# Performance work log

Hardware: AMD Instinct MI355X
Metric: run time of the kernel (lower is better)

Reference implementation:

```python
import jax, jax.numpy as jnp
import numpy as np
from jax import lax

FS = 250
FREQS = np.arange(1.0, 41.0)  # 40 frequencies, 1..40 Hz
NCH = 32
NCYC = 6.0

def _kernel_size():
    f_min = float(FREQS.min())
    cyc = max(2.0, NCYC * (f_min / 4.0)) if f_min < 4.0 else NCYC
    sigma_max = cyc / (2.0 * np.pi * f_min)
    K = int(8 * sigma_max * FS)
    if K % 2 == 0:
        K += 1
    return K

def _morlet_weights():
    K = _kernel_size()
    t = np.linspace(-K / 2 / FS, K / 2 / FS, K)
    w = np.zeros((len(FREQS), 2, K), dtype=np.float32)
    for i, f in enumerate(FREQS):
        if f < 1.0:
            cycles = 3.0 + f * (4.0 - 3.0)
        elif f < 4.0:
            cycles = 4.0 + (f - 1.0) / 3.0 * (6.0 - 4.0)
        else:
            cycles = NCYC
        sigma = cycles / (2.0 * np.pi * f)
        wav = np.exp(2j * np.pi * f * t) * np.exp(-t ** 2 / (2 * sigma ** 2))
        wav = wav / np.linalg.norm(wav)
        w[i, 0] = np.real(wav)
        w[i, 1] = np.imag(wav)
    # per-channel layout: [f0_real, f0_imag, f1_real, ...] repeated for each of NCH groups
    W = np.tile(w[None], (NCH, 1, 1, 1)).reshape(NCH * len(FREQS) * 2, 1, K)
    return jnp.asarray(W)

# fixed 7x5 electrode grid mapping (channels 0..31)
_MAP = np.array([[-1, 0, -1, 1, -1], [2, 3, 4, 5, 6], [7, 8, 13, 9, 10],
                 [11, 12, 18, 14, 15], [16, 17, 19, 20, 21],
                 [22, 23, 24, 25, 26], [27, 28, 29, 30, 31]])
ROWS = np.array([np.where(_MAP == c)[0][0] for c in range(32)])
COLS = np.array([np.where(_MAP == c)[1][0] for c in range(32)])


def setup_inputs() -> dict:
    key = jax.random.key(0)
    x = jax.random.normal(key, (8, 32, 2000), dtype=jnp.float32)
    return {"x": x, "W": _morlet_weights()}


def reference(x, W):
    B, C, T = x.shape
    F = W.shape[0] // (C * 2)
    pad = W.shape[-1] // 2
    # reflect padding (padding_mode='reflect') then VALID grouped conv (groups=C)
    xp = jnp.pad(x, ((0, 0), (0, 0), (pad, pad)), mode='reflect')
    y = lax.conv_general_dilated(
        xp, W, window_strides=(1,), padding='VALID',
        dimension_numbers=('NCH', 'OIH', 'NCH'), feature_group_count=C)
    y = y.reshape(B, C, F, 2, T)
    real = y[:, :, :, 0, :]
    imag = y[:, :, :, 1, :]
    mag = jnp.sqrt(real * real + imag * imag)
    phase = jnp.arctan2(imag, real)
    features = jnp.stack([mag, phase], axis=-1)          # [B, C, F, T, 2]
    features = jnp.transpose(features, (0, 4, 2, 1, 3))  # [B, 2, F, C, T]
    canvas = jnp.zeros((B, 2, F, 7, 5, T), dtype=x.dtype)
    canvas = canvas.at[:, :, :, ROWS, COLS, :].set(features)  # [B, 2, F, 7, 5, T]
    return canvas
```

## Files before the change

kernel.cpp:

```cpp
#include <hip/hip_runtime.h>
#include <math.h>

#define NB 8
#define NC 32
#define NF 40
#define NT 2000
#define KW 637
#define PADW 318
#define TPB 256
#define HALFT 1000
#define XPN 1680
#define FG 4
#define NFG (NF / FG)

#define XSIZE (NB * NC * NT)
#define KC 320

#define DET  3e-4f
#define DET2 1e-7f

__device__ __constant__ int POS[32] = {
  1,3,5,6,7,8,9,10,11,13,14,15,16,12,18,19,20,21,17,22,23,24,25,26,
  27,28,29,30,31,32,33,34
};

__global__ __launch_bounds__(TPB)
void cwt_zero_holes(float* __restrict__ out) {
  int row = blockIdx.x;
  int p = (row % 3) * 2;
  int rest = row / 3;
  size_t base = ((size_t)rest * 35 + p) * NT;
  float4 z = make_float4(0.f, 0.f, 0.f, 0.f);
  for (int t = threadIdx.x * 4; t < NT; t += TPB * 4)
    *(float4*)&out[base + t] = z;
}

__device__ __noinline__ float2 fixup_point(const float* __restrict__ xv,
                                           const float* __restrict__ wr,
                                           const float* __restrict__ wi) {
  float b0r = 0.f, b0i = 0.f;
  #pragma unroll 4
  for (int k = 0; k < KC; ++k) {
    const float v = xv[k];
    b0r = __fadd_rn(b0r, __fmul_rn(wr[k], v));
    b0i = __fadd_rn(b0i, __fmul_rn(wi[k], v));
  }
  float b1r = 0.f, b1i = 0.f;
  #pragma unroll 4
  for (int k = KC; k < KW; ++k) {
    const float v = xv[k];
    b1r = __fadd_rn(b1r, __fmul_rn(wr[k], v));
    b1i = __fadd_rn(b1i, __fmul_rn(wi[k], v));
  }
  const float re = __fadd_rn(b0r, b1r);
  const float im = __fadd_rn(b0i, b1i);
  return make_float2(sqrtf(__fadd_rn(__fmul_rn(re, re), __fmul_rn(im, im))),
                     atan2f(im, re));
}

__global__ __launch_bounds__(TPB)
void cwt_fast(const float* __restrict__ x,
              const float* __restrict__ W,
              float* __restrict__ out) {
  __shared__ __align__(16) float xp[XPN];

  const int bid  = blockIdx.x;
  const int g    = bid & (FG - 1);
  const int half = (bid >> 2) & 1;
  const int bc   = bid >> 3;
  const int b    = bc >> 5;
  const int c    = bc & 31;
  const int tid  = threadIdx.x;

  const float* __restrict__ xrow = x + (size_t)(b * NC + c) * NT;
  const int gbase = half * HALFT;

  for (int i = tid; i < XPN; i += TPB) {
    int m = gbase + i - PADW;
    if (m < 0) m = -m;
    if (m >= NT) m = 2 * NT - 2 - m;
    xp[i] = xrow[m];
  }
  __syncthreads();

  const int t_loc = tid * 4;
  const bool active = (t_loc < HALFT);
  const int t_glob = gbase + t_loc;
  const int pos = POS[c];

  for (int j = 0; j < NFG; ++j) {
    const int fi = g + FG * j;
    const float* __restrict__ wr_g = W + (size_t)(2 * fi) * KW;
    const float* __restrict__ wi_g = wr_g + KW;

    const float cyc = (fi == 0) ? 4.0f
                    : (fi == 1) ? (4.0f + 2.0f / 3.0f)
                    : (fi == 2) ? (4.0f + 4.0f / 3.0f) : 6.0f;
    const float sigma = cyc / (6.283185307179586f * (float)(fi + 1));
    int h = (int)ceilf(6.0f * sigma * 250.0f);
    if (h > PADW) h = PADW;
    const int k_lo  = (PADW - h) & ~3;
    const int k_end = PADW + h + 1;
    const int nsteps = (k_end - k_lo + 3) >> 2;

    float re[4] = {0.f, 0.f, 0.f, 0.f};
    float im[4] = {0.f, 0.f, 0.f, 0.f};

    float4 cur = *(const float4*)&xp[t_loc + k_lo];
    int ks = k_lo;
    for (int s = 0; s < nsteps - 1; ++s, ks += 4) {
      const float4 nxt = *(const float4*)&xp[t_loc + ks + 4];
      const float wrA[4] = {wr_g[ks], wr_g[ks+1], wr_g[ks+2], wr_g[ks+3]};
      const float wiA[4] = {wi_g[ks], wi_g[ks+1], wi_g[ks+2], wi_g[ks+3]};
      float v[8] = {cur.x, cur.y, cur.z, cur.w, nxt.x, nxt.y, nxt.z, nxt.w};
      #pragma unroll
      for (int u = 0; u < 4; ++u) {
        #pragma unroll
        for (int jj = 0; jj < 4; ++jj) {
          re[jj] = __fmaf_rn(v[u + jj], wrA[u], re[jj]);
          im[jj] = __fmaf_rn(v[u + jj], wiA[u], im[jj]);
        }
      }
      cur = nxt;
    }
    {
      const float4 nxt = *(const float4*)&xp[t_loc + ks + 4];
      float wrA[4], wiA[4];
      #pragma unroll
      for (int u = 0; u < 4; ++u) {
        const bool in = (ks + u) < k_end;
        wrA[u] = in ? wr_g[ks + u] : 0.f;
        wiA[u] = in ? wi_g[ks + u] : 0.f;
      }
      float v[8] = {cur.x, cur.y, cur.z, cur.w, nxt.x, nxt.y, nxt.z, nxt.w};
      #pragma unroll
      for (int u = 0; u < 4; ++u) {
        #pragma unroll
        for (int jj = 0; jj < 4; ++jj) {
          re[jj] = __fmaf_rn(v[u + jj], wrA[u], re[jj]);
          im[jj] = __fmaf_rn(v[u + jj], wiA[u], im[jj]);
        }
      }
    }

    if (active) {
      float4 mag, ph;
      mag.x = sqrtf(re[0]*re[0] + im[0]*im[0]);
      mag.y = sqrtf(re[1]*re[1] + im[1]*im[1]);
      mag.z = sqrtf(re[2]*re[2] + im[2]*im[2]);
      mag.w = sqrtf(re[3]*re[3] + im[3]*im[3]);
      ph.x = atan2f(im[0], re[0]);
      ph.y = atan2f(im[1], re[1]);
      ph.z = atan2f(im[2], re[2]);
      ph.w = atan2f(im[3], re[3]);

      float* mp = &mag.x;
      float* pp = &ph.x;
      #pragma unroll
      for (int jj = 0; jj < 4; ++jj) {
        const float a = re[jj], bb = im[jj];
        if ((fabsf(bb) < DET && a < 0.f) || (a * a + bb * bb < DET2)) {
          float2 r = fixup_point(xp + t_loc + jj, wr_g, wi_g);
          mp[jj] = r.x; pp[jj] = r.y;
        }
      }

      const size_t magbase = ((size_t)((2*b + 0) * NF + fi) * 35 + pos) * NT;
      const size_t phbase  = ((size_t)((2*b + 1) * NF + fi) * 35 + pos) * NT;
      *(float4*)&out[magbase + t_glob] = mag;
      *(float4*)&out[phbase  + t_glob] = ph;
    }
  }
}

extern "C" void kernel_launch(void* const* d_in, const int* in_sizes, int n_in,
                              void* d_out, int out_size, void* d_ws, size_t ws_size,
                              hipStream_t stream) {
  const void* xin = d_in[0];
  const void* win = (n_in > 1) ? d_in[1] : d_in[0];
  if (n_in >= 2) {
    if (in_sizes[0] == XSIZE)      { xin = d_in[0]; win = d_in[1]; }
    else if (in_sizes[1] == XSIZE) { xin = d_in[1]; win = d_in[0]; }
  }
  const float* x = (const float*)xin;
  const float* W = (const float*)win;
  float* out = (float*)d_out;

  cwt_zero_holes<<<dim3(NB * 2 * NF * 3), dim3(TPB), 0, stream>>>(out);
  cwt_fast<<<dim3(NB * NC * 2 * FG), dim3(TPB), 0, stream>>>(x, W, out);
}
```

Measured before the change: 572.3 us.

## Stage wavelet taps in LDS and compute two time halves per thread

Each block now covers the full 2000-sample row instead of half, and each thread accumulates two output quads (t and t+1000), so every weight load is reused across twice as many outputs. The trimmed, zero-padded wavelet taps for the block's frequency group are staged once into shared memory and read as float4, replacing the scalar global weight loads. The grid is halved, which lowers parallelism to 1024 blocks with only 250 active threads each. Register pressure and LDS use per block both go up.

Result: no change. 583.1 us (+1.9%).

```diff
diff --git a/kernel.cpp b/kernel.cpp
--- a/kernel.cpp
+++ b/kernel.cpp
@@ -9,7 +9,9 @@
 #define PADW 318
 #define TPB 256
 #define HALFT 1000
-#define XPN 1680
+#define XLN  (NT + 2 * PADW)
+#define XLNP 2656
+#define WMAX 5120
 #define FG 4
 #define NFG (NF / FG)
 
@@ -58,117 +60,159 @@
                      atan2f(im, re));
 }
 
+__device__ __forceinline__ void support_window(int fi, int& klo, int& kend,
+                                               int& Lp) {
+  const float cyc = (fi == 0) ? 4.0f
+                  : (fi == 1) ? (4.0f + 2.0f / 3.0f)
+                  : (fi == 2) ? (4.0f + 4.0f / 3.0f) : 6.0f;
+  const float sigma = cyc / (6.283185307179586f * (float)(fi + 1));
+  int h = (int)ceilf(6.0f * sigma * 250.0f);
+  if (h > PADW) h = PADW;
+  klo  = (PADW - h) & ~3;
+  kend = PADW + h + 1;
+  Lp   = (kend - klo + 3) & ~3;
+}
+
 __global__ __launch_bounds__(TPB)
 void cwt_fast(const float* __restrict__ x,
               const float* __restrict__ W,
               float* __restrict__ out) {
-  __shared__ __align__(16) float xp[XPN];
-
-  const int bid  = blockIdx.x;
-  const int g    = bid & (FG - 1);
-  const int half = (bid >> 2) & 1;
-  const int bc   = bid >> 3;
-  const int b    = bc >> 5;
-  const int c    = bc & 31;
-  const int tid  = threadIdx.x;
+  __shared__ __align__(16) float xp[XLNP];
+  __shared__ __align__(16) float wlds[WMAX];
+
+  const int bid = blockIdx.x;
+  const int g   = bid & (FG - 1);
+  const int bc  = bid >> 2;
+  const int b   = bc >> 5;
+  const int c   = bc & 31;
+  const int tid = threadIdx.x;
 
   const float* __restrict__ xrow = x + (size_t)(b * NC + c) * NT;
-  const int gbase = half * HALFT;
-
-  for (int i = tid; i < XPN; i += TPB) {
-    int m = gbase + i - PADW;
-    if (m < 0) m = -m;
-    if (m >= NT) m = 2 * NT - 2 - m;
-    xp[i] = xrow[m];
+
+  for (int i = tid; i < XLNP; i += TPB) {
+    float v = 0.f;
+    if (i < XLN) {
+      int s = i - PADW;
+      int m = (s < 0) ? -s : ((s >= NT) ? (2 * NT - 2 - s) : s);
+      v = xrow[m];
+    }
+    xp[i] = v;
+  }
+
+  {
+    int woff = 0;
+    for (int j = 0; j < NFG; ++j) {
+      const int fi = g + FG * j;
+      int klo, kend, Lp;
+      support_window(fi, klo, kend, Lp);
+      const float* __restrict__ wr_g = W + (size_t)(2 * fi) * KW;
+      const float* __restrict__ wi_g = wr_g + KW;
+      for (int i = tid; i < Lp; i += TPB) {
+        const int k = klo + i;
+        const bool in = k < kend;
+        wlds[woff + i]      = in ? wr_g[k] : 0.f;
+        wlds[woff + Lp + i] = in ? wi_g[k] : 0.f;
+      }
+      woff += 2 * Lp;
+    }
   }
   __syncthreads();
 
-  const int t_loc = tid * 4;
-  const bool active = (t_loc < HALFT);
-  const int t_glob = gbase + t_loc;
+  const bool active = (tid < HALFT / 4);
+  const int ta = tid * 4;
+  const int tb = tid * 4 + HALFT;
   const int pos = POS[c];
-
+  const float4* __restrict__ xp4 = (const float4*)xp;
+
+  int woff = 0;
   for (int j = 0; j < NFG; ++j) {
     const int fi = g + FG * j;
-    const float* __restrict__ wr_g = W + (size_t)(2 * fi) * KW;
-    const float* __restrict__ wi_g = wr_g + KW;
-
-    const float cyc = (fi == 0) ? 4.0f
-                    : (fi == 1) ? (4.0f + 2.0f / 3.0f)
-                    : (fi == 2) ? (4.0f + 4.0f / 3.0f) : 6.0f;
-    const float sigma = cyc / (6.283185307179586f * (float)(fi + 1));
-    int h = (int)ceilf(6.0f * sigma * 250.0f);
-    if (h > PADW) h = PADW;
-    const int k_lo  = (PADW - h) & ~3;
-    const int k_end = PADW + h + 1;
-    const int nsteps = (k_end - k_lo + 3) >> 2;
-
-    float re[4] = {0.f, 0.f, 0.f, 0.f};
-    float im[4] = {0.f, 0.f, 0.f, 0.f};
-
-    float4 cur = *(const float4*)&xp[t_loc + k_lo];
-    int ks = k_lo;
-    for (int s = 0; s < nsteps - 1; ++s, ks += 4) {
-      const float4 nxt = *(const float4*)&xp[t_loc + ks + 4];
-      const float wrA[4] = {wr_g[ks], wr_g[ks+1], wr_g[ks+2], wr_g[ks+3]};
-      const float wiA[4] = {wi_g[ks], wi_g[ks+1], wi_g[ks+2], wi_g[ks+3]};
-      float v[8] = {cur.x, cur.y, cur.z, cur.w, nxt.x, nxt.y, nxt.z, nxt.w};
+    int klo, kend, Lp;
+    support_window(fi, klo, kend, Lp);
+    const float* __restrict__ wr = wlds + woff;
+    const float* __restrict__ wi = wr + Lp;
+    woff += 2 * Lp;
+    if (!active) continue;
+
+    const int nst = Lp >> 2;
+    const int ia0 = (ta + klo) >> 2;
+    const int ib0 = (tb + klo) >> 2;
+    float4 a0 = xp4[ia0], a1 = xp4[ia0 + 1];
+    float4 b0 = xp4[ib0], b1 = xp4[ib0 + 1];
+
+    float rea[4] = {0.f,0.f,0.f,0.f}, ima[4] = {0.f,0.f,0.f,0.f};
+    float reb[4] = {0.f,0.f,0.f,0.f}, imb[4] = {0.f,0.f,0.f,0.f};
+
+    for (int s = 0; s < nst; ++s) {
+      const float4 wr4 = ((const float4*)wr)[s];
+      const float4 wi4 = ((const float4*)wi)[s];
+      const float4 a2 = xp4[ia0 + s + 2];
+      const float4 b2 = xp4[ib0 + s + 2];
+      const float va[8] = {a0.x,a0.y,a0.z,a0.w, a1.x,a1.y,a1.z,a1.w};
+      const float vb[8] = {b0.x,b0.y,b0.z,b0.w, b1.x,b1.y,b1.z,b1.w};
+      const float wrA[4] = {wr4.x, wr4.y, wr4.z, wr4.w};
+      const float wiA[4] = {wi4.x, wi4.y, wi4.z, wi4.w};
       #pragma unroll
       for (int u = 0; u < 4; ++u) {
         #pragma unroll
-        for (int jj = 0; jj < 4; ++jj) {
-          re[jj] = __fmaf_rn(v[u + jj], wrA[u], re[jj]);
-          im[jj] = __fmaf_rn(v[u + jj], wiA[u], im[jj]);
+        for (int q = 0; q < 4; ++q) {
+          rea[q] = __fmaf_rn(va[u + q], wrA[u], rea[q]);
+          ima[q] = __fmaf_rn(va[u + q], wiA[u], ima[q]);
+          reb[q] = __fmaf_rn(vb[u + q], wrA[u], reb[q]);
+          imb[q] = __fmaf_rn(vb[u + q], wiA[u], imb[q]);
         }
       }
-      cur = nxt;
-    }
+      a0 = a1; a1 = a2; b0 = b1; b1 = b2;
+    }
+
+    const size_t magbase = ((size_t)((2*b + 0) * NF + fi) * 35 + pos) * NT;
+    const size_t phbase  = ((size_t)((2*b + 1) * NF + fi) * 35 + pos) * NT;
+    const float* __restrict__ wr_gf = W + (size_t)(2 * fi) * KW;
+    const float* __restrict__ wi_gf = wr_gf + KW;
+
     {
-      const float4 nxt = *(const float4*)&xp[t_loc + ks + 4];
-      float wrA[4], wiA[4];
+      float4 mag, ph;
+      float* mp = &mag.x; float* pp = &ph.x;
+      mag.x = sqrtf(rea[0]*rea[0] + ima[0]*ima[0]);
+      mag.y = sqrtf(rea[1]*rea[1] + ima[1]*ima[1]);
+      mag.z = sqrtf(rea[2]*rea[2] + ima[2]*ima[2]);
+      mag.w = sqrtf(rea[3]*rea[3] + ima[3]*ima[3]);
+      ph.x = atan2f(ima[0], rea[0]);
+      ph.y = atan2f(ima[1], rea[1]);
+      ph.z = atan2f(ima[2], rea[2]);
+      ph.w = atan2f(ima[3], rea[3]);
       #pragma unroll
-      for (int u = 0; u < 4; ++u) {
-        const bool in = (ks + u) < k_end;
-        wrA[u] = in ? wr_g[ks + u] : 0.f;
-        wiA[u] = in ? wi_g[ks + u] : 0.f;
-      }
-      float v[8] = {cur.x, cur.y, cur.z, cur.w, nxt.x, nxt.y, nxt.z, nxt.w};
+      for (int q = 0; q < 4; ++q) {
+        const float a = rea[q], bb = ima[q];
+        if ((fabsf(bb) < DET && a < 0.f) || (a * a + bb * bb < DET2)) {
+          float2 r = fixup_point(xp + ta + q, wr_gf, wi_gf);
+          mp[q] = r.x; pp[q] = r.y;
+        }
+      }
+      *(float4*)&out[magbase + ta] = mag;
+      *(float4*)&out[phbase  + ta] = ph;
+    }
+    {
+      float4 mag, ph;
+      float* mp = &mag.x; float* pp = &ph.x;
+      mag.x = sqrtf(reb[0]*reb[0] + imb[0]*imb[0]);
+      mag.y = sqrtf(reb[1]*reb[1] + imb[1]*imb[1]);
+      mag.z = sqrtf(reb[2]*reb[2] + imb[2]*imb[2]);
+      mag.w = sqrtf(reb[3]*reb[3] + imb[3]*imb[3]);
+      ph.x = atan2f(imb[0], reb[0]);
+      ph.y = atan2f(imb[1], reb[1]);
+      ph.z = atan2f(imb[2], reb[2]);
+      ph.w = atan2f(imb[3], reb[3]);
       #pragma unroll
-      for (int u = 0; u < 4; ++u) {
-        #pragma unroll
-        for (int jj = 0; jj < 4; ++jj) {
-          re[jj] = __fmaf_rn(v[u + jj], wrA[u], re[jj]);
-          im[jj] = __fmaf_rn(v[u + jj], wiA[u], im[jj]);
+      for (int q = 0; q < 4; ++q) {
+        const float a = reb[q], bb = imb[q];
+        if ((fabsf(bb) < DET && a < 0.f) || (a * a + bb * bb < DET2)) {
+          float2 r = fixup_point(xp + tb + q, wr_gf, wi_gf);
+          mp[q] = r.x; pp[q] = r.y;
         }
       }
-    }
-
-    if (active) {
-      float4 mag, ph;
-      mag.x = sqrtf(re[0]*re[0] + im[0]*im[0]);
-      mag.y = sqrtf(re[1]*re[1] + im[1]*im[1]);
-      mag.z = sqrtf(re[2]*re[2] + im[2]*im[2]);
-      mag.w = sqrtf(re[3]*re[3] + im[3]*im[3]);
-      ph.x = atan2f(im[0], re[0]);
-      ph.y = atan2f(im[1], re[1]);
-      ph.z = atan2f(im[2], re[2]);
-      ph.w = atan2f(im[3], re[3]);
-
-      float* mp = &mag.x;
-      float* pp = &ph.x;
-      #pragma unroll
-      for (int jj = 0; jj < 4; ++jj) {
-        const float a = re[jj], bb = im[jj];
-        if ((fabsf(bb) < DET && a < 0.f) || (a * a + bb * bb < DET2)) {
-          float2 r = fixup_point(xp + t_loc + jj, wr_g, wi_g);
-          mp[jj] = r.x; pp[jj] = r.y;
-        }
-      }
-
-      const size_t magbase = ((size_t)((2*b + 0) * NF + fi) * 35 + pos) * NT;
-      const size_t phbase  = ((size_t)((2*b + 1) * NF + fi) * 35 + pos) * NT;
-      *(float4*)&out[magbase + t_glob] = mag;
-      *(float4*)&out[phbase  + t_glob] = ph;
+      *(float4*)&out[magbase + tb] = mag;
+      *(float4*)&out[phbase  + tb] = ph;
     }
   }
 }
@@ -187,5 +231,5 @@
   float* out = (float*)d_out;
 
   cwt_zero_holes<<<dim3(NB * 2 * NF * 3), dim3(TPB), 0, stream>>>(out);
-  cwt_fast<<<dim3(NB * NC * 2 * FG), dim3(TPB), 0, stream>>>(x, W, out);
-}
+  cwt_fast<<<dim3(NB * NC * FG), dim3(TPB), 0, stream>>>(x, W, out);
+}
```
